# Kernel tuning notes

Measured on AMD Instinct MI355X. Metric: run time of the kernel, lower is better.

## Reference

```python
import jax, jax.numpy as jnp
import numpy as np
from jax import lax

H = 512
V = 32000
B = 64
S = 64
T = 32
TQ = 32
NUM_HOP = 3


def _p(key, shape, scale=0.05):
    return jax.random.normal(key, shape, dtype=jnp.float32) * scale


def setup_inputs() -> dict:
    key = jax.random.key(0)
    ks = jax.random.split(key, 20)
    inp = {}
    inp["contexts"] = jax.random.randint(ks[0], (B, S, T), 0, V)
    inp["questions"] = jax.random.randint(ks[1], (B, TQ), 0, V)
    inp["emb"] = _p(ks[2], (V, H), 1.0)
    # input module: bidirectional GRU (torch gate order r,z,n)
    inp["Wih_f"] = _p(ks[3], (3 * H, H)); inp["Whh_f"] = _p(ks[4], (3 * H, H))
    inp["bih_f"] = jnp.zeros((3 * H,), jnp.float32); inp["bhh_f"] = jnp.zeros((3 * H,), jnp.float32)
    inp["Wih_b"] = _p(ks[5], (3 * H, H)); inp["Whh_b"] = _p(ks[6], (3 * H, H))
    inp["bih_b"] = jnp.zeros((3 * H,), jnp.float32); inp["bhh_b"] = jnp.zeros((3 * H,), jnp.float32)
    # question module GRU
    inp["qWih"] = _p(ks[7], (3 * H, H)); inp["qWhh"] = _p(ks[8], (3 * H, H))
    inp["qbih"] = jnp.zeros((3 * H,), jnp.float32); inp["qbhh"] = jnp.zeros((3 * H,), jnp.float32)
    # attention GRU cell (note: source reuses br as both biases)
    inp["Wr"] = _p(ks[9], (H, H)); inp["Ur"] = _p(ks[10], (H, H)); inp["br"] = jnp.ones((H,), jnp.float32)
    inp["W"] = _p(ks[11], (H, H)); inp["U"] = _p(ks[12], (H, H))
    # episodic memory gate MLP + next-memory projection
    inp["z1_w"] = _p(ks[13], (H, 4 * H)); inp["z1_b"] = jnp.zeros((H,), jnp.float32)
    inp["z2_w"] = _p(ks[14], (1, H)); inp["z2_b"] = jnp.zeros((1,), jnp.float32)
    inp["nm_w"] = _p(ks[15], (H, 3 * H)); inp["nm_b"] = jnp.zeros((H,), jnp.float32)
    # answer module
    inp["ans_w"] = _p(ks[16], (V, 2 * H)); inp["ans_b"] = jnp.zeros((V,), jnp.float32)
    return inp


def _pos_enc(slen, elen):
    # l[s, e] = 1 - s/slen - (e/elen)*(1 - 2*s/slen); indexed by SENTENCE dim, as in source
    s = np.arange(slen, dtype=np.float64)[:, None]
    e = np.arange(elen, dtype=np.float64)[None, :]
    l = 1.0 - s / slen - (e / elen) * (1.0 - 2.0 * s / slen)
    return jnp.asarray(l, dtype=jnp.float32)  # (S, H)


def _gru(x, Wih, Whh, bih, bhh, reverse=False):
    # x: (B, T, H); torch nn.GRU math with gate order r, z, n
    Bn, Tn, Hn = x.shape
    h0 = jnp.zeros((Bn, Hn), x.dtype)

    def step(h, xt):
        gx = xt @ Wih.T + bih
        gh = h @ Whh.T + bhh
        xr, xz, xn = jnp.split(gx, 3, axis=-1)
        hr, hz, hn = jnp.split(gh, 3, axis=-1)
        r = jax.nn.sigmoid(xr + hr)
        z = jax.nn.sigmoid(xz + hz)
        n = jnp.tanh(xn + r * hn)
        h_new = (1.0 - z) * n + z * h
        return h_new, h_new

    h_last, hs = lax.scan(step, h0, jnp.swapaxes(x, 0, 1), reverse=reverse)
    return jnp.swapaxes(hs, 0, 1), h_last


def _dmn(emb, Wih_f, Whh_f, bih_f, bhh_f, Wih_b, Whh_b, bih_b, bhh_b,
         qWih, qWhh, qbih, qbhh, Wr, Ur, br, W, U,
         z1_w, z1_b, z2_w, z2_b, nm_w, nm_b, ans_w, ans_b,
         contexts, questions):
    emb0 = emb.at[0].set(0.0)  # padding_idx=0
    Bn, Sn, Tn = contexts.shape
    Hn = emb.shape[1]
    # ---- input module ----
    ce = emb0[contexts]                                   # (B,S,T,H)
    pe = _pos_enc(Sn, Hn)                                 # (S,H), broadcast over tokens (faithful)
    facts_in = jnp.sum(ce * pe[None, :, None, :], axis=2)  # (B,S,H)
    hf, _ = _gru(facts_in, Wih_f, Whh_f, bih_f, bhh_f, reverse=False)
    hb, _ = _gru(facts_in, Wih_b, Whh_b, bih_b, bhh_b, reverse=True)
    facts = hf + hb                                       # (B,S,H); dropout = identity (eval)
    # ---- question module ----
    _, q = _gru(emb0[questions], qWih, qWhh, qbih, qbhh)  # (B,H)
    # ---- episodic memory hops ----
    facts_t = jnp.swapaxes(facts, 0, 1)                   # (S,B,H)
    M = q
    for _ in range(NUM_HOP):
        qb = q[:, None, :]
        Mb = M[:, None, :]
        z = jnp.concatenate([facts * qb, facts * Mb,
                             jnp.abs(facts - qb), jnp.abs(facts - Mb)], axis=-1)  # (B,S,4H)
        g1 = jnp.tanh(z @ z1_w.T + z1_b)
        G = jax.nn.softmax((g1 @ z2_w.T + z2_b)[..., 0], axis=1)  # (B,S)

        def agru(c, sg):
            fact, g = sg
            r = jax.nn.sigmoid(fact @ Wr + c @ Ur + br)
            ht = jnp.tanh(fact @ W + r * (c @ U) + br)  # source reuses br as b
            return g[:, None] * ht + (1.0 - g[:, None]) * c, None

        C, _ = lax.scan(agru, jnp.zeros((Bn, Hn), facts.dtype), (facts_t, G.T))
        M = jax.nn.relu(jnp.concatenate([M, C, q], axis=-1) @ nm_w.T + nm_b)
    # ---- answer module (dropout = identity) ----
    preds = jnp.concatenate([M, q], axis=-1) @ ans_w.T + ans_b  # (B,V)
    return preds


def reference(contexts, questions, emb, Wih_f, Whh_f, bih_f, bhh_f,
              Wih_b, Whh_b, bih_b, bhh_b, qWih, qWhh, qbih, qbhh,
              Wr, Ur, br, W, U, z1_w, z1_b, z2_w, z2_b, nm_w, nm_b,
              ans_w, ans_b):
    return _dmn(emb, Wih_f, Whh_f, bih_f, bhh_f, Wih_b, Whh_b, bih_b, bhh_b,
                qWih, qWhh, qbih, qbhh, Wr, Ur, br, W, U,
                z1_w, z1_b, z2_w, z2_b, nm_w, nm_b, ans_w, ans_b,
                contexts, questions)
```

## Files before the change

kernel.cpp:

```cpp
#include <hip/hip_runtime.h>
#include <cstddef>
#include <cstdint>

namespace {

constexpr int H  = 512;
constexpr int V  = 32000;
constexpr int B  = 64;
constexpr int S  = 64;
constexpr int T  = 32;
constexpr int TQ = 32;

typedef unsigned short ushort_t;
typedef __attribute__((ext_vector_type(8))) short bf16x8;
typedef __attribute__((ext_vector_type(4))) short bf16x4;
typedef __attribute__((ext_vector_type(4))) float f32x4;

__device__ __forceinline__ ushort_t f2bf(float f) {
  union { float f; unsigned u; } v; v.f = f;
  return (ushort_t)((v.u + 0x7FFFu + ((v.u >> 16) & 1u)) >> 16);
}

__device__ __forceinline__ float sigm(float x) { return 1.f / (1.f + expf(-x)); }

__device__ __forceinline__ bf16x8 pack8(f32x4 a, f32x4 b) {
  bf16x8 r;
  r[0] = (short)f2bf(a.x); r[1] = (short)f2bf(a.y);
  r[2] = (short)f2bf(a.z); r[3] = (short)f2bf(a.w);
  r[4] = (short)f2bf(b.x); r[5] = (short)f2bf(b.y);
  r[6] = (short)f2bf(b.z); r[7] = (short)f2bf(b.w);
  return r;
}
__device__ __forceinline__ bf16x4 pack4(f32x4 a) {
  bf16x4 r;
  r[0] = (short)f2bf(a.x); r[1] = (short)f2bf(a.y);
  r[2] = (short)f2bf(a.z); r[3] = (short)f2bf(a.w);
  return r;
}

__device__ __forceinline__ f32x4 load4c(const float* p) {
  f32x4 v;
  asm volatile("global_load_dwordx4 %0, %1, off sc0 sc1" : "=v"(v) : "v"(p));
  return v;
}
__device__ __forceinline__ float load1c(const float* p) {
  float v;
  asm volatile("global_load_dword %0, %1, off sc0 sc1" : "=v"(v) : "v"(p));
  return v;
}
__device__ __forceinline__ void store1c(float* p, float v) {
  asm volatile("global_store_dword %0, %1, off sc0 sc1" :: "v"(p), "v"(v) : "memory");
}
__device__ __forceinline__ void waitvm0() {
  asm volatile("s_waitcnt vmcnt(0)" ::: "memory");
  __builtin_amdgcn_sched_barrier(0);
}

__device__ __forceinline__ void group_barrier_nc(unsigned* cell, unsigned target) {
  waitvm0();
  __syncthreads();
  if (threadIdx.x == 0) {
    __hip_atomic_fetch_add(cell, 1u, __ATOMIC_RELAXED, __HIP_MEMORY_SCOPE_AGENT);
    unsigned v;
    do {
      v = __hip_atomic_load(cell, __ATOMIC_RELAXED, __HIP_MEMORY_SCOPE_AGENT);
      if (v < target) __builtin_amdgcn_s_sleep(2);
    } while (v < target);
  }
  __syncthreads();
}

__global__ __launch_bounds__(256) void k_embed_facts(const int* __restrict__ ctx,
                                                     const float* __restrict__ emb,
                                                     float* __restrict__ facts_in) {
  const int bs = blockIdx.x;
  const int s  = bs & (S - 1);
  const int t  = threadIdx.x;
  __shared__ int sidx[T];
  if (t < T) sidx[t] = ctx[(size_t)bs * T + t];
  __syncthreads();
  float a0 = 0.f, a1 = 0.f;
  for (int tt = 0; tt < T; ++tt) {
    const int ix = sidx[tt];
    if (ix != 0) {
      const float* e = emb + ((size_t)ix << 9);
      a0 += e[t];
      a1 += e[t + 256];
    }
  }
  const float sf = (float)s * (1.f / 64.f);
  const float c1 = 1.f - sf;
  const float c2 = (1.f - 2.f * sf) * (1.f / 512.f);
  facts_in[((size_t)bs << 9) + t]       = a0 * (c1 - (float)t * c2);
  facts_in[((size_t)bs << 9) + t + 256] = a1 * (c1 - (float)(t + 256) * c2);
}

__global__ __launch_bounds__(256) void k_embed_q(const int* __restrict__ qidx,
                                                 const float* __restrict__ emb,
                                                 float* __restrict__ qe) {
  const int bt = blockIdx.x;
  const int t  = threadIdx.x;
  const int ix = qidx[bt];
  float v0 = 0.f, v1 = 0.f;
  if (ix != 0) {
    const float* e = emb + ((size_t)ix << 9);
    v0 = e[t];
    v1 = e[t + 256];
  }
  qe[((size_t)bt << 9) + t]       = v0;
  qe[((size_t)bt << 9) + t + 256] = v1;
}

__global__ __launch_bounds__(256) void k_transpose512(const float* __restrict__ src,
                                                      float* __restrict__ dst) {
  __shared__ float tile[32][33];
  const int x0 = blockIdx.x * 32, y0 = blockIdx.y * 32;
  for (int i = threadIdx.y; i < 32; i += 8)
    tile[i][threadIdx.x] = src[(size_t)(y0 + i) * H + x0 + threadIdx.x];
  __syncthreads();
  for (int i = threadIdx.y; i < 32; i += 8)
    dst[(size_t)(x0 + i) * H + y0 + threadIdx.x] = tile[threadIdx.x][i];
}

template <bool A_BF16, int ACT>
__global__ __launch_bounds__(256) void k_gemm_mfma(const void* __restrict__ Av,
                                                   const float* __restrict__ Bm,
                                                   const float* __restrict__ bias,
                                                   float* __restrict__ C,
                                                   int M, int N, int K) {
  __shared__ __align__(16) ushort_t As[64][72];
  __shared__ __align__(16) ushort_t Bs[64][72];
  const int t    = threadIdx.x;
  const int lane = t & 63;
  const int w    = t >> 6;
  const int wr   = w >> 1, wc = w & 1;
  const int m0 = blockIdx.y << 6, n0 = blockIdx.x << 6;
  const int row = t >> 2;
  const int ch  = t & 3;

  f32x4 acc[2][2] = {};

  for (int k0 = 0; k0 < K; k0 += 64) {
    if (A_BF16) {
      const ushort_t* A16 = (const ushort_t*)Av;
#pragma unroll
      for (int cc = 0; cc < 2; ++cc) {
        const int c8 = ch + cc * 4;
        const uint4 v = *(const uint4*)(A16 + (size_t)(m0 + row) * K + k0 + c8 * 8);
        *(uint4*)&As[row][c8 * 8] = v;
      }
    } else {
      const float* Af = (const float*)Av;
#pragma unroll
      for (int cc = 0; cc < 2; ++cc) {
        const int c8 = ch + cc * 4;
        const float* src = Af + (size_t)(m0 + row) * K + k0 + c8 * 8;
        const f32x4 f0 = *(const f32x4*)src;
        const f32x4 f1 = *(const f32x4*)(src + 4);
        *(bf16x8*)&As[row][c8 * 8] = pack8(f0, f1);
      }
    }
    {
#pragma unroll
      for (int cc = 0; cc < 2; ++cc) {
        const int c8 = ch + cc * 4;
        const float* src = Bm + (size_t)(n0 + row) * K + k0 + c8 * 8;
        const f32x4 f0 = *(const f32x4*)src;
        const f32x4 f1 = *(const f32x4*)(src + 4);
        *(bf16x8*)&Bs[row][c8 * 8] = pack8(f0, f1);
      }
    }
    __syncthreads();
#pragma unroll
    for (int ks = 0; ks < 2; ++ks) {
      bf16x8 a[2], b[2];
#pragma unroll
      for (int fr = 0; fr < 2; ++fr)
        a[fr] = *(const bf16x8*)&As[wr * 32 + fr * 16 + (lane & 15)][ks * 32 + (lane >> 4) * 8];
#pragma unroll
      for (int fc = 0; fc < 2; ++fc)
        b[fc] = *(const bf16x8*)&Bs[wc * 32 + fc * 16 + (lane & 15)][ks * 32 + (lane >> 4) * 8];
#pragma unroll
      for (int fr = 0; fr < 2; ++fr)
#pragma unroll
        for (int fc = 0; fc < 2; ++fc)
          acc[fr][fc] = __builtin_amdgcn_mfma_f32_16x16x32_bf16(a[fr], b[fc], acc[fr][fc], 0, 0, 0);
    }
    __syncthreads();
  }
#pragma unroll
  for (int fr = 0; fr < 2; ++fr) {
#pragma unroll
    for (int fc = 0; fc < 2; ++fc) {
      const int rbase = m0 + wr * 32 + fr * 16 + ((lane >> 4) << 2);
      const int col   = n0 + wc * 32 + fc * 16 + (lane & 15);
      const float bv  = bias ? bias[col] : 0.f;
#pragma unroll
      for (int j = 0; j < 4; ++j) {
        float v = acc[fr][fc][j] + bv;
        if (ACT == 1) v = tanhf(v);
        if (ACT == 2) v = fmaxf(v, 0.f);
        C[(size_t)(rbase + j) * N + col] = v;
      }
    }
  }
}

__global__ __launch_bounds__(256, 1) void k_gru_scan_mfma(
    const float* __restrict__ Whh_f, const float* __restrict__ bhh_f,
    const float* __restrict__ Whh_b, const float* __restrict__ bhh_b,
    const float* __restrict__ qWhh,  const float* __restrict__ qbhh,
    const float* __restrict__ gx_f, const float* __restrict__ gx_b,
    const float* __restrict__ gx_q,
    float* __restrict__ Hbuf, float* __restrict__ facts,
    float* __restrict__ hb_all, unsigned* __restrict__ bar) {
  const int bx   = blockIdx.x;
  const int grp  = bx >> 3;
  const int rank = bx & 7;
  const int gru  = grp >> 2;
  const int ib   = grp & 3;

  const float* Whh; const float* bhh; const float* gx;
  float* H0; float* H1; float* out_seq; int seqlen, rev;
  if (gru == 0)      { Whh = Whh_f; bhh = bhh_f; gx = gx_f; H0 = Hbuf;          H1 = Hbuf + 32768;  out_seq = facts;   seqlen = S;  rev = 0; }
  else if (gru == 1) { Whh = Whh_b; bhh = bhh_b; gx = gx_b; H0 = Hbuf + 65536;  H1 = Hbuf + 98304;  out_seq = hb_all;  seqlen = S;  rev = 1; }
  else               { Whh = qWhh;  bhh = qbhh;  gx = gx_q; H0 = Hbuf + 131072; H1 = Hbuf + 163840; out_seq = nullptr; seqlen = TQ; rev = 0; }

  __shared__ __align__(16) ushort_t hl[16 * 520];

  const int t    = threadIdx.x;
  const int lane = t & 63;
  const int wv   = t >> 6;
  const int nt   = (rank << 2) + wv;
  const int lm   = lane & 15;
  const int lk   = lane >> 4;
  const int col  = (nt << 4) + lm;

  bf16x8 wf[3][16];
#pragma unroll
  for (int g = 0; g < 3; ++g) {
    const float* wrow = Whh + ((size_t)(g * 512 + col) << 9) + (lk << 3);
#pragma unroll
    for (int ks = 0; ks < 16; ++ks) {
      const float* p = wrow + ks * 32;
      wf[g][ks] = pack8(*(const f32x4*)p, *(const f32x4*)(p + 4));
    }
  }
  const float bv0 = bhh[col], bv1 = bhh[512 + col], bv2 = bhh[1024 + col];
  unsigned* cell = bar + grp * 64;
  unsigned tgt = 0;

  for (int s = 0; s < seqlen; ++s) {
    const int xidx = rev ? (seqlen - 1 - s) : s;
    float xr[4], xz[4], xn[4];
#pragma unroll
    for (int j = 0; j < 4; ++j) {
      const int b = (ib << 4) + (lk << 2) + j;
      const size_t gxrow = ((size_t)b * seqlen + xidx) * 1536;
      xr[j] = gx[gxrow + col];
      xz[j] = gx[gxrow + 512 + col];
      xn[j] = gx[gxrow + 1024 + col];
    }

    float hp[4] = {0.f, 0.f, 0.f, 0.f};
    if (s == 0) {
      for (int i = t; i < 4160; i += 256) ((unsigned*)hl)[i] = 0u;
    } else {
      const float* Hp = (s & 1) ? H1 : H0;
      f32x4 v[8];
#pragma unroll
      for (int u = 0; u < 8; ++u) {
        const int i = (u << 8) + t;
        v[u] = load4c(Hp + ((size_t)((ib << 4) + (i >> 7)) << 9) + ((i & 127) << 2));
      }
#pragma unroll
      for (int j = 0; j < 4; ++j)
        hp[j] = load1c(Hp + ((size_t)((ib << 4) + (lk << 2) + j) << 9) + col);
      waitvm0();
#pragma unroll
      for (int u = 0; u < 8; ++u) {
        const int i = (u << 8) + t;
        *(bf16x4*)&hl[(i >> 7) * 520 + ((i & 127) << 2)] = pack4(v[u]);
      }
    }
    __syncthreads();

    f32x4 acc0 = {}, acc1 = {}, acc2 = {};
#pragma unroll
    for (int ks = 0; ks < 16; ++ks) {
      const bf16x8 a = *(const bf16x8*)&hl[lm * 520 + (ks << 5) + (lk << 3)];
      acc0 = __builtin_amdgcn_mfma_f32_16x16x32_bf16(a, wf[0][ks], acc0, 0, 0, 0);
      acc1 = __builtin_amdgcn_mfma_f32_16x16x32_bf16(a, wf[1][ks], acc1, 0, 0, 0);
      acc2 = __builtin_amdgcn_mfma_f32_16x16x32_bf16(a, wf[2][ks], acc2, 0, 0, 0);
    }

    float* Hn = (s & 1) ? H0 : H1;
#pragma unroll
    for (int j = 0; j < 4; ++j) {
      const int b = (ib << 4) + (lk << 2) + j;
      const float r = sigm(xr[j] + acc0[j] + bv0);
      const float z = sigm(xz[j] + acc1[j] + bv1);
      const float n = tanhf(xn[j] + r * (acc2[j] + bv2));
      const float hnew = (1.f - z) * n + z * hp[j];
      store1c(Hn + ((size_t)b << 9) + col, hnew);
      if (out_seq) out_seq[((size_t)(b * S + xidx) << 9) + col] = hnew;
    }
    if (s + 1 < seqlen) {
      tgt += 8;
      group_barrier_nc(cell, tgt);
    }
  }
}

__global__ __launch_bounds__(256, 1) void k_agru_scan_mfma(
    const float* __restrict__ UrT, const float* __restrict__ UT,
    const float* __restrict__ fRW, const float* __restrict__ fW,
    const float* __restrict__ br, const float* __restrict__ G,
    float* __restrict__ C0, float* __restrict__ C1,
    unsigned* __restrict__ bar) {
  const int bx   = blockIdx.x;
  const int grp  = bx >> 3;
  const int rank = bx & 7;

  __shared__ __align__(16) ushort_t cl[16 * 520];

  const int t    = threadIdx.x;
  const int lane = t & 63;
  const int wv   = t >> 6;
  const int nt   = (rank << 2) + wv;
  const int lm   = lane & 15;
  const int lk   = lane >> 4;
  const int col  = (nt << 4) + lm;

  bf16x8 wfr[16], wfu[16];
  {
    const float* r0 = UrT + ((size_t)col << 9) + (lk << 3);
    const float* r1 = UT  + ((size_t)col << 9) + (lk << 3);
#pragma unroll
    for (int ks = 0; ks < 16; ++ks) {
      wfr[ks] = pack8(*(const f32x4*)(r0 + ks * 32), *(const f32x4*)(r0 + ks * 32 + 4));
      wfu[ks] = pack8(*(const f32x4*)(r1 + ks * 32), *(const f32x4*)(r1 + ks * 32 + 4));
    }
  }
  const float brv = br[col];
  unsigned* cell = bar + grp * 64;
  unsigned tgt = 0;

  for (int s = 0; s < S; ++s) {
    float fr[4], fw[4], gg[4];
#pragma unroll
    for (int j = 0; j < 4; ++j) {
      const int b = (grp << 4) + (lk << 2) + j;
      const size_t fi = ((size_t)(b * S + s) << 9) + col;
      fr[j] = fRW[fi];
      fw[j] = fW[fi];
      gg[j] = G[(b << 6) + s];
    }

    float cp[4] = {0.f, 0.f, 0.f, 0.f};
    if (s == 0) {
      for (int i = t; i < 4160; i += 256) ((unsigned*)cl)[i] = 0u;
    } else {
      const float* Cp = (s & 1) ? C1 : C0;
      f32x4 v[8];
#pragma unroll
      for (int u = 0; u < 8; ++u) {
        const int i = (u << 8) + t;
        v[u] = load4c(Cp + ((size_t)((grp << 4) + (i >> 7)) << 9) + ((i & 127) << 2));
      }
#pragma unroll
      for (int j = 0; j < 4; ++j)
        cp[j] = load1c(Cp + ((size_t)((grp << 4) + (lk << 2) + j) << 9) + col);
      waitvm0();
#pragma unroll
      for (int u = 0; u < 8; ++u) {
        const int i = (u << 8) + t;
        *(bf16x4*)&cl[(i >> 7) * 520 + ((i & 127) << 2)] = pack4(v[u]);
      }
    }
    __syncthreads();

    f32x4 accr = {}, accu = {};
#pragma unroll
    for (int ks = 0; ks < 16; ++ks) {
      const bf16x8 a = *(const bf16x8*)&cl[lm * 520 + (ks << 5) + (lk << 3)];
      accr = __builtin_amdgcn_mfma_f32_16x16x32_bf16(a, wfr[ks], accr, 0, 0, 0);
      accu = __builtin_amdgcn_mfma_f32_16x16x32_bf16(a, wfu[ks], accu, 0, 0, 0);
    }

    float* Cn = (s & 1) ? C0 : C1;
#pragma unroll
    for (int j = 0; j < 4; ++j) {
      const int b = (grp << 4) + (lk << 2) + j;
      const float r  = sigm(fr[j] + accr[j] + brv);
      const float ht = tanhf(fw[j] + r * accu[j] + brv);
      store1c(Cn + ((size_t)b << 9) + col, gg[j] * ht + (1.f - gg[j]) * cp[j]);
    }
    if (s + 1 < S) {
      tgt += 8;
      group_barrier_nc(cell, tgt);
    }
  }
}

__global__ __launch_bounds__(256) void k_add(float* __restrict__ a, const float* __restrict__ b) {
  const size_t i = (((size_t)blockIdx.x << 8) + threadIdx.x) << 2;
  float4 x = *(float4*)(a + i);
  const float4 y = *(const float4*)(b + i);
  x.x += y.x; x.y += y.y; x.z += y.z; x.w += y.w;
  *(float4*)(a + i) = x;
}

__global__ __launch_bounds__(256) void k_build_z16(const float* __restrict__ facts,
                                                   const float* __restrict__ q,
                                                   const float* __restrict__ M,
                                                   ushort_t* __restrict__ z) {
  const int bs = blockIdx.x;
  const int b  = bs >> 6;
  const int t  = threadIdx.x;
  const size_t zb = (size_t)bs << 11;
  for (int c = t; c < 512; c += 256) {
    const float f  = facts[((size_t)bs << 9) + c];
    const float qv = q[(b << 9) + c];
    const float mv = M[(b << 9) + c];
    z[zb + c]        = f2bf(f * qv);
    z[zb + 512 + c]  = f2bf(f * mv);
    z[zb + 1024 + c] = f2bf(fabsf(f - qv));
    z[zb + 1536 + c] = f2bf(fabsf(f - mv));
  }
}

__global__ __launch_bounds__(256) void k_score_softmax(const float* __restrict__ g1,
                                                       const float* __restrict__ z2w,
                                                       const float* __restrict__ z2b,
                                                       float* __restrict__ G) {
  const int b = blockIdx.x, t = threadIdx.x;
  const int wave = t >> 6, lane = t & 63;
  __shared__ float sc[64];
  for (int si = 0; si < 16; ++si) {
    const int s = wave * 16 + si;
    const float* row = g1 + ((size_t)(b * S + s) << 9) + lane * 8;
    const float* w   = z2w + lane * 8;
    float p = 0.f;
#pragma unroll
    for (int k = 0; k < 8; ++k) p += row[k] * w[k];
#pragma unroll
    for (int off = 32; off; off >>= 1) p += __shfl_xor(p, off);
    if (lane == 0) sc[s] = p + z2b[0];
  }
  __syncthreads();
  if (wave == 0) {
    const float v = sc[lane];
    float m = v;
#pragma unroll
    for (int off = 32; off; off >>= 1) m = fmaxf(m, __shfl_xor(m, off));
    const float e = expf(v - m);
    float su = e;
#pragma unroll
    for (int off = 32; off; off >>= 1) su += __shfl_xor(su, off);
    G[(b << 6) + lane] = e / su;
  }
}

__global__ __launch_bounds__(256) void k_concat3(const float* __restrict__ M,
                                                 const float* __restrict__ C,
                                                 const float* __restrict__ q,
                                                 float* __restrict__ out) {
  const int b = blockIdx.x, t = threadIdx.x;
  for (int c = t; c < 512; c += 256) {
    out[(size_t)b * 1536 + c]        = M[(b << 9) + c];
    out[(size_t)b * 1536 + 512 + c]  = C[(b << 9) + c];
    out[(size_t)b * 1536 + 1024 + c] = q[(b << 9) + c];
  }
}

__global__ __launch_bounds__(256) void k_concat2(const float* __restrict__ M,
                                                 const float* __restrict__ q,
                                                 float* __restrict__ out) {
  const int b = blockIdx.x, t = threadIdx.x;
  for (int c = t; c < 512; c += 256) {
    out[(size_t)b * 1024 + c]       = M[(b << 9) + c];
    out[(size_t)b * 1024 + 512 + c] = q[(b << 9) + c];
  }
}

}

extern "C" void kernel_launch(void* const* d_in, const int* in_sizes, int n_in,
                              void* d_out, int out_size, void* d_ws, size_t ws_size,
                              hipStream_t stream) {
  const int*   contexts  = (const int*)d_in[0];
  const int*   questions = (const int*)d_in[1];
  const float* emb   = (const float*)d_in[2];
  const float* Wih_f = (const float*)d_in[3];
  const float* Whh_f = (const float*)d_in[4];
  const float* bih_f = (const float*)d_in[5];
  const float* bhh_f = (const float*)d_in[6];
  const float* Wih_b = (const float*)d_in[7];
  const float* Whh_b = (const float*)d_in[8];
  const float* bih_b = (const float*)d_in[9];
  const float* bhh_b = (const float*)d_in[10];
  const float* qWih  = (const float*)d_in[11];
  const float* qWhh  = (const float*)d_in[12];
  const float* qbih  = (const float*)d_in[13];
  const float* qbhh  = (const float*)d_in[14];
  const float* Wr    = (const float*)d_in[15];
  const float* Ur    = (const float*)d_in[16];
  const float* br    = (const float*)d_in[17];
  const float* Wm    = (const float*)d_in[18];
  const float* Um    = (const float*)d_in[19];
  const float* z1_w  = (const float*)d_in[20];
  const float* z1_b  = (const float*)d_in[21];
  const float* z2_w  = (const float*)d_in[22];
  const float* z2_b  = (const float*)d_in[23];
  const float* nm_w  = (const float*)d_in[24];
  const float* nm_b  = (const float*)d_in[25];
  const float* ans_w = (const float*)d_in[26];
  const float* ans_b = (const float*)d_in[27];
  (void)in_sizes; (void)n_in; (void)out_size; (void)ws_size;

  float* ws = (float*)d_ws;
  float* WrT      = ws + 0;
  float* UrT      = ws + 262144;
  float* WT       = ws + 524288;
  float* UT       = ws + 786432;
  float* facts_in = ws + 1048576;
  float* qe       = ws + 3145728;
  float* gx_f     = ws + 4194304;
  float* gx_b     = ws + 10485760;
  float* gx_q     = ws + 16777216;
  float* facts    = ws + 19922944;
  float* hb       = ws + 22020096;
  float* Hbuf     = ws + 24117248;
  float* C0       = ws + 24313856;
  float* C1       = ws + 24346624;
  float* M0       = ws + 24379392;
  float* M1       = ws + 24412160;
  float* MCq      = ws + 24444928;
  float* Mq       = ws + 24543232;
  float* Gm       = ws + 24608768;
  ushort_t* zb16 = (ushort_t*)gx_f;
  float* g1  = gx_q;
  float* fRW = facts_in;
  float* fW  = hb;
  float* preds = (float*)d_out;
  unsigned* bar = (unsigned*)Mq;

  float* Hq0 = Hbuf + 131072;
  float* q = Hq0;

  hipMemsetAsync(bar, 0, 48 * 64 * sizeof(unsigned), stream);

  k_embed_facts<<<B * S, 256, 0, stream>>>(contexts, emb, facts_in);
  k_embed_q<<<B * TQ, 256, 0, stream>>>(questions, emb, qe);
  dim3 tb(32, 8);
  k_transpose512<<<dim3(16, 16), tb, 0, stream>>>(Wr, WrT);
  k_transpose512<<<dim3(16, 16), tb, 0, stream>>>(Ur, UrT);
  k_transpose512<<<dim3(16, 16), tb, 0, stream>>>(Wm, WT);
  k_transpose512<<<dim3(16, 16), tb, 0, stream>>>(Um, UT);

  k_gemm_mfma<false, 0><<<dim3(24, 64), 256, 0, stream>>>(facts_in, Wih_f, bih_f, gx_f, 4096, 1536, 512);
  k_gemm_mfma<false, 0><<<dim3(24, 64), 256, 0, stream>>>(facts_in, Wih_b, bih_b, gx_b, 4096, 1536, 512);
  k_gemm_mfma<false, 0><<<dim3(24, 32), 256, 0, stream>>>(qe, qWih, qbih, gx_q, 2048, 1536, 512);

  k_gru_scan_mfma<<<96, 256, 0, stream>>>(Whh_f, bhh_f, Whh_b, bhh_b, qWhh, qbhh,
                                          gx_f, gx_b, gx_q, Hbuf, facts, hb, bar);
  k_add<<<2048, 256, 0, stream>>>(facts, hb);

  k_gemm_mfma<false, 0><<<dim3(8, 64), 256, 0, stream>>>(facts, WrT, nullptr, fRW, 4096, 512, 512);
  k_gemm_mfma<false, 0><<<dim3(8, 64), 256, 0, stream>>>(facts, WT,  nullptr, fW,  4096, 512, 512);

  const float* Mcur = q;
  for (int h = 0; h < 3; ++h) {
    k_build_z16<<<B * S, 256, 0, stream>>>(facts, q, Mcur, zb16);
    k_gemm_mfma<true, 1><<<dim3(8, 64), 256, 0, stream>>>(zb16, z1_w, z1_b, g1, 4096, 512, 2048);
    k_score_softmax<<<B, 256, 0, stream>>>(g1, z2_w, z2_b, Gm);
    {
      unsigned* ba = bar + (24 + h * 8) * 64;
      k_agru_scan_mfma<<<32, 256, 0, stream>>>(UrT, UT, fRW, fW, br, Gm, C0, C1, ba);
    }
    k_concat3<<<B, 256, 0, stream>>>(Mcur, C0, q, MCq);
    float* Mnext = (h & 1) ? M1 : M0;
    k_gemm_mfma<false, 2><<<dim3(8, 1), 256, 0, stream>>>(MCq, nm_w, nm_b, Mnext, 64, 512, 1536);
    Mcur = Mnext;
  }

  k_concat2<<<B, 256, 0, stream>>>(Mcur, q, Mq);
  k_gemm_mfma<false, 0><<<dim3(500, 1), 256, 0, stream>>>(Mq, ans_w, ans_b, preds, 64, 32000, 1024);
}
```

Measured before the change: 1.462 ms.

## Use per-rank flag barriers, prefetch next-step inputs, fuse concat/z-build into GEMMs

Replaces the atomic-counter group barrier in both GRU scans with per-rank flag stores polled by one wavefront, which removes contended atomics on the serial critical path. Next-step gate inputs are loaded before the barrier so their latency overlaps the wait. The z-feature build, concat3 and concat2 kernels are folded into specialized GEMM loaders, cutting launches and intermediate buffers. The trade-off is that z1 now recomputes the elementwise features per N-tile.

```diff
diff --git a/kernel.cpp b/kernel.cpp
--- a/kernel.cpp
+++ b/kernel.cpp
@@ -25,16 +25,16 @@
 
 __device__ __forceinline__ bf16x8 pack8(f32x4 a, f32x4 b) {
   bf16x8 r;
-  r[0] = (short)f2bf(a.x); r[1] = (short)f2bf(a.y);
-  r[2] = (short)f2bf(a.z); r[3] = (short)f2bf(a.w);
-  r[4] = (short)f2bf(b.x); r[5] = (short)f2bf(b.y);
-  r[6] = (short)f2bf(b.z); r[7] = (short)f2bf(b.w);
+  r[0] = (short)f2bf(a[0]); r[1] = (short)f2bf(a[1]);
+  r[2] = (short)f2bf(a[2]); r[3] = (short)f2bf(a[3]);
+  r[4] = (short)f2bf(b[0]); r[5] = (short)f2bf(b[1]);
+  r[6] = (short)f2bf(b[2]); r[7] = (short)f2bf(b[3]);
   return r;
 }
 __device__ __forceinline__ bf16x4 pack4(f32x4 a) {
   bf16x4 r;
-  r[0] = (short)f2bf(a.x); r[1] = (short)f2bf(a.y);
-  r[2] = (short)f2bf(a.z); r[3] = (short)f2bf(a.w);
+  r[0] = (short)f2bf(a[0]); r[1] = (short)f2bf(a[1]);
+  r[2] = (short)f2bf(a[2]); r[3] = (short)f2bf(a[3]);
   return r;
 }
 
@@ -51,21 +51,29 @@
 __device__ __forceinline__ void store1c(float* p, float v) {
   asm volatile("global_store_dword %0, %1, off sc0 sc1" :: "v"(p), "v"(v) : "memory");
 }
+__device__ __forceinline__ void store1cu(unsigned* p, unsigned v) {
+  asm volatile("global_store_dword %0, %1, off sc0 sc1" :: "v"(p), "v"(v) : "memory");
+}
 __device__ __forceinline__ void waitvm0() {
   asm volatile("s_waitcnt vmcnt(0)" ::: "memory");
   __builtin_amdgcn_sched_barrier(0);
 }
 
-__device__ __forceinline__ void group_barrier_nc(unsigned* cell, unsigned target) {
+__device__ __forceinline__ void flag_barrier(unsigned* flags, int rank,
+                                             unsigned step1, int t, int lane, int wv) {
   waitvm0();
   __syncthreads();
-  if (threadIdx.x == 0) {
-    __hip_atomic_fetch_add(cell, 1u, __ATOMIC_RELAXED, __HIP_MEMORY_SCOPE_AGENT);
-    unsigned v;
-    do {
-      v = __hip_atomic_load(cell, __ATOMIC_RELAXED, __HIP_MEMORY_SCOPE_AGENT);
-      if (v < target) __builtin_amdgcn_s_sleep(2);
-    } while (v < target);
+  if (t == 0) store1cu(flags + rank * 32, step1);
+  if (wv == 0) {
+    const unsigned* fp = flags + (lane & 7) * 32;
+    for (;;) {
+      unsigned v;
+      asm volatile("global_load_dword %0, %1, off sc0 sc1" : "=v"(v) : "v"(fp));
+      asm volatile("s_waitcnt vmcnt(0)" ::: "memory");
+      const int ok = (lane >= 8) || (v >= step1);
+      if (__all(ok)) break;
+      __builtin_amdgcn_s_sleep(1);
+    }
   }
   __syncthreads();
 }
@@ -122,8 +130,8 @@
     dst[(size_t)(x0 + i) * H + y0 + threadIdx.x] = tile[threadIdx.x][i];
 }
 
-template <bool A_BF16, int ACT>
-__global__ __launch_bounds__(256) void k_gemm_mfma(const void* __restrict__ Av,
+template <int ACT>
+__global__ __launch_bounds__(256) void k_gemm_mfma(const float* __restrict__ Af,
                                                    const float* __restrict__ Bm,
                                                    const float* __restrict__ bias,
                                                    float* __restrict__ C,
@@ -141,34 +149,13 @@
   f32x4 acc[2][2] = {};
 
   for (int k0 = 0; k0 < K; k0 += 64) {
-    if (A_BF16) {
-      const ushort_t* A16 = (const ushort_t*)Av;
-#pragma unroll
-      for (int cc = 0; cc < 2; ++cc) {
-        const int c8 = ch + cc * 4;
-        const uint4 v = *(const uint4*)(A16 + (size_t)(m0 + row) * K + k0 + c8 * 8);
-        *(uint4*)&As[row][c8 * 8] = v;
-      }
-    } else {
-      const float* Af = (const float*)Av;
-#pragma unroll
-      for (int cc = 0; cc < 2; ++cc) {
-        const int c8 = ch + cc * 4;
-        const float* src = Af + (size_t)(m0 + row) * K + k0 + c8 * 8;
-        const f32x4 f0 = *(const f32x4*)src;
-        const f32x4 f1 = *(const f32x4*)(src + 4);
-        *(bf16x8*)&As[row][c8 * 8] = pack8(f0, f1);
-      }
-    }
-    {
-#pragma unroll
-      for (int cc = 0; cc < 2; ++cc) {
-        const int c8 = ch + cc * 4;
-        const float* src = Bm + (size_t)(n0 + row) * K + k0 + c8 * 8;
-        const f32x4 f0 = *(const f32x4*)src;
-        const f32x4 f1 = *(const f32x4*)(src + 4);
-        *(bf16x8*)&Bs[row][c8 * 8] = pack8(f0, f1);
-      }
+#pragma unroll
+    for (int cc = 0; cc < 2; ++cc) {
+      const int c8 = ch + cc * 4;
+      const float* src = Af + (size_t)(m0 + row) * K + k0 + c8 * 8;
+      *(bf16x8*)&As[row][c8 * 8] = pack8(*(const f32x4*)src, *(const f32x4*)(src + 4));
+      const float* srb = Bm + (size_t)(n0 + row) * K + k0 + c8 * 8;
+      *(bf16x8*)&Bs[row][c8 * 8] = pack8(*(const f32x4*)srb, *(const f32x4*)(srb + 4));
     }
     __syncthreads();
 #pragma unroll
@@ -202,6 +189,207 @@
         if (ACT == 2) v = fmaxf(v, 0.f);
         C[(size_t)(rbase + j) * N + col] = v;
       }
+    }
+  }
+}
+
+__global__ __launch_bounds__(256) void k_gemm_z1(const float* __restrict__ facts,
+                                                 const float* __restrict__ qv,
+                                                 const float* __restrict__ Mv,
+                                                 const float* __restrict__ Bm,
+                                                 const float* __restrict__ bias,
+                                                 float* __restrict__ C) {
+  constexpr int N = 512, K = 2048;
+  __shared__ __align__(16) ushort_t As[64][72];
+  __shared__ __align__(16) ushort_t Bs[64][72];
+  const int t    = threadIdx.x;
+  const int lane = t & 63;
+  const int w    = t >> 6;
+  const int wr   = w >> 1, wc = w & 1;
+  const int m0 = blockIdx.y << 6, n0 = blockIdx.x << 6;
+  const int row = t >> 2;
+  const int ch  = t & 3;
+  const int b   = blockIdx.y;
+
+  f32x4 acc[2][2] = {};
+
+  for (int k0 = 0; k0 < K; k0 += 64) {
+    const int seg = k0 >> 9;
+    const int kb  = k0 & 511;
+    const float* other = ((seg & 1) ? Mv : qv) + ((size_t)b << 9);
+#pragma unroll
+    for (int cc = 0; cc < 2; ++cc) {
+      const int c8 = ch + cc * 4;
+      const int kk = kb + c8 * 8;
+      const float* fp = facts + ((size_t)(m0 + row) << 9) + kk;
+      const f32x4 f0 = *(const f32x4*)fp;
+      const f32x4 f1 = *(const f32x4*)(fp + 4);
+      const f32x4 o0 = *(const f32x4*)(other + kk);
+      const f32x4 o1 = *(const f32x4*)(other + kk + 4);
+      f32x4 z0, z1;
+      if (seg < 2) {
+        z0 = f0 * o0; z1 = f1 * o1;
+      } else {
+        z0 = f0 - o0; z1 = f1 - o1;
+#pragma unroll
+        for (int e = 0; e < 4; ++e) { z0[e] = fabsf(z0[e]); z1[e] = fabsf(z1[e]); }
+      }
+      *(bf16x8*)&As[row][c8 * 8] = pack8(z0, z1);
+      const float* srb = Bm + (size_t)(n0 + row) * K + k0 + c8 * 8;
+      *(bf16x8*)&Bs[row][c8 * 8] = pack8(*(const f32x4*)srb, *(const f32x4*)(srb + 4));
+    }
+    __syncthreads();
+#pragma unroll
+    for (int ks = 0; ks < 2; ++ks) {
+      bf16x8 a[2], bb[2];
+#pragma unroll
+      for (int fr = 0; fr < 2; ++fr)
+        a[fr] = *(const bf16x8*)&As[wr * 32 + fr * 16 + (lane & 15)][ks * 32 + (lane >> 4) * 8];
+#pragma unroll
+      for (int fc = 0; fc < 2; ++fc)
+        bb[fc] = *(const bf16x8*)&Bs[wc * 32 + fc * 16 + (lane & 15)][ks * 32 + (lane >> 4) * 8];
+#pragma unroll
+      for (int fr = 0; fr < 2; ++fr)
+#pragma unroll
+        for (int fc = 0; fc < 2; ++fc)
+          acc[fr][fc] = __builtin_amdgcn_mfma_f32_16x16x32_bf16(a[fr], bb[fc], acc[fr][fc], 0, 0, 0);
+    }
+    __syncthreads();
+  }
+#pragma unroll
+  for (int fr = 0; fr < 2; ++fr) {
+#pragma unroll
+    for (int fc = 0; fc < 2; ++fc) {
+      const int rbase = m0 + wr * 32 + fr * 16 + ((lane >> 4) << 2);
+      const int col   = n0 + wc * 32 + fc * 16 + (lane & 15);
+      const float bv  = bias[col];
+#pragma unroll
+      for (int j = 0; j < 4; ++j)
+        C[(size_t)(rbase + j) * N + col] = tanhf(acc[fr][fc][j] + bv);
+    }
+  }
+}
+
+__global__ __launch_bounds__(256) void k_gemm_cat3(const float* __restrict__ Mv,
+                                                   const float* __restrict__ Cv,
+                                                   const float* __restrict__ qv,
+                                                   const float* __restrict__ Bm,
+                                                   const float* __restrict__ bias,
+                                                   float* __restrict__ C) {
+  constexpr int N = 512, K = 1536;
+  __shared__ __align__(16) ushort_t As[64][72];
+  __shared__ __align__(16) ushort_t Bs[64][72];
+  const int t    = threadIdx.x;
+  const int lane = t & 63;
+  const int w    = t >> 6;
+  const int wr   = w >> 1, wc = w & 1;
+  const int n0 = blockIdx.x << 6;
+  const int row = t >> 2;
+  const int ch  = t & 3;
+
+  f32x4 acc[2][2] = {};
+
+  for (int k0 = 0; k0 < K; k0 += 64) {
+    const int seg = k0 >> 9;
+    const float* src = (seg == 0) ? Mv : (seg == 1) ? Cv : qv;
+    const int kb = k0 & 511;
+#pragma unroll
+    for (int cc = 0; cc < 2; ++cc) {
+      const int c8 = ch + cc * 4;
+      const float* fp = src + ((size_t)row << 9) + kb + c8 * 8;
+      *(bf16x8*)&As[row][c8 * 8] = pack8(*(const f32x4*)fp, *(const f32x4*)(fp + 4));
+      const float* srb = Bm + (size_t)(n0 + row) * K + k0 + c8 * 8;
+      *(bf16x8*)&Bs[row][c8 * 8] = pack8(*(const f32x4*)srb, *(const f32x4*)(srb + 4));
+    }
+    __syncthreads();
+#pragma unroll
+    for (int ks = 0; ks < 2; ++ks) {
+      bf16x8 a[2], bb[2];
+#pragma unroll
+      for (int fr = 0; fr < 2; ++fr)
+        a[fr] = *(const bf16x8*)&As[wr * 32 + fr * 16 + (lane & 15)][ks * 32 + (lane >> 4) * 8];
+#pragma unroll
+      for (int fc = 0; fc < 2; ++fc)
+        bb[fc] = *(const bf16x8*)&Bs[wc * 32 + fc * 16 + (lane & 15)][ks * 32 + (lane >> 4) * 8];
+#pragma unroll
+      for (int fr = 0; fr < 2; ++fr)
+#pragma unroll
+        for (int fc = 0; fc < 2; ++fc)
+          acc[fr][fc] = __builtin_amdgcn_mfma_f32_16x16x32_bf16(a[fr], bb[fc], acc[fr][fc], 0, 0, 0);
+    }
+    __syncthreads();
+  }
+#pragma unroll
+  for (int fr = 0; fr < 2; ++fr) {
+#pragma unroll
+    for (int fc = 0; fc < 2; ++fc) {
+      const int rbase = wr * 32 + fr * 16 + ((lane >> 4) << 2);
+      const int col   = n0 + wc * 32 + fc * 16 + (lane & 15);
+      const float bv  = bias[col];
+#pragma unroll
+      for (int j = 0; j < 4; ++j)
+        C[(size_t)(rbase + j) * N + col] = fmaxf(acc[fr][fc][j] + bv, 0.f);
+    }
+  }
+}
+
+__global__ __launch_bounds__(256) void k_gemm_cat2(const float* __restrict__ Mv,
+                                                   const float* __restrict__ qv,
+                                                   const float* __restrict__ Bm,
+                                                   const float* __restrict__ bias,
+                                                   float* __restrict__ C) {
+  constexpr int N = 32000, K = 1024;
+  __shared__ __align__(16) ushort_t As[64][72];
+  __shared__ __align__(16) ushort_t Bs[64][72];
+  const int t    = threadIdx.x;
+  const int lane = t & 63;
+  const int w    = t >> 6;
+  const int wr   = w >> 1, wc = w & 1;
+  const int n0 = blockIdx.x << 6;
+  const int row = t >> 2;
+  const int ch  = t & 3;
+
+  f32x4 acc[2][2] = {};
+
+  for (int k0 = 0; k0 < K; k0 += 64) {
+    const float* src = (k0 < 512) ? Mv : qv;
+    const int kb = k0 & 511;
+#pragma unroll
+    for (int cc = 0; cc < 2; ++cc) {
+      const int c8 = ch + cc * 4;
+      const float* fp = src + ((size_t)row << 9) + kb + c8 * 8;
+      *(bf16x8*)&As[row][c8 * 8] = pack8(*(const f32x4*)fp, *(const f32x4*)(fp + 4));
+      const float* srb = Bm + (size_t)(n0 + row) * K + k0 + c8 * 8;
+      *(bf16x8*)&Bs[row][c8 * 8] = pack8(*(const f32x4*)srb, *(const f32x4*)(srb + 4));
+    }
+    __syncthreads();
+#pragma unroll
+    for (int ks = 0; ks < 2; ++ks) {
+      bf16x8 a[2], bb[2];
+#pragma unroll
+      for (int fr = 0; fr < 2; ++fr)
+        a[fr] = *(const bf16x8*)&As[wr * 32 + fr * 16 + (lane & 15)][ks * 32 + (lane >> 4) * 8];
+#pragma unroll
+      for (int fc = 0; fc < 2; ++fc)
+        bb[fc] = *(const bf16x8*)&Bs[wc * 32 + fc * 16 + (lane & 15)][ks * 32 + (lane >> 4) * 8];
+#pragma unroll
+      for (int fr = 0; fr < 2; ++fr)
+#pragma unroll
+        for (int fc = 0; fc < 2; ++fc)
+          acc[fr][fc] = __builtin_amdgcn_mfma_f32_16x16x32_bf16(a[fr], bb[fc], acc[fr][fc], 0, 0, 0);
+    }
+    __syncthreads();
+  }
+#pragma unroll
+  for (int fr = 0; fr < 2; ++fr) {
+#pragma unroll
+    for (int fc = 0; fc < 2; ++fc) {
+      const int rbase = wr * 32 + fr * 16 + ((lane >> 4) << 2);
+      const int col   = n0 + wc * 32 + fc * 16 + (lane & 15);
+      const float bv  = bias[col];
+#pragma unroll
+      for (int j = 0; j < 4; ++j)
+        C[(size_t)(rbase + j) * N + col] = acc[fr][fc][j] + bv;
     }
   }
 }
@@ -213,7 +401,7 @@
     const float* __restrict__ gx_f, const float* __restrict__ gx_b,
     const float* __restrict__ gx_q,
     float* __restrict__ Hbuf, float* __restrict__ facts,
-    float* __restrict__ hb_all, unsigned* __restrict__ bar) {
+    float* __restrict__ hb_all, unsigned* __restrict__ flags_base) {
   const int bx   = blockIdx.x;
   const int grp  = bx >> 3;
   const int rank = bx & 7;
@@ -247,12 +435,11 @@
     }
   }
   const float bv0 = bhh[col], bv1 = bhh[512 + col], bv2 = bhh[1024 + col];
-  unsigned* cell = bar + grp * 64;
-  unsigned tgt = 0;
-
-  for (int s = 0; s < seqlen; ++s) {
-    const int xidx = rev ? (seqlen - 1 - s) : s;
-    float xr[4], xz[4], xn[4];
+  unsigned* flags = flags_base + grp * 8 * 32;
+
+  float xr[4], xz[4], xn[4];
+  {
+    const int xidx = rev ? (seqlen - 1) : 0;
 #pragma unroll
     for (int j = 0; j < 4; ++j) {
       const int b = (ib << 4) + (lk << 2) + j;
@@ -261,7 +448,9 @@
       xz[j] = gx[gxrow + 512 + col];
       xn[j] = gx[gxrow + 1024 + col];
     }
-
+  }
+
+  for (int s = 0; s < seqlen; ++s) {
     float hp[4] = {0.f, 0.f, 0.f, 0.f};
     if (s == 0) {
       for (int i = t; i < 4160; i += 256) ((unsigned*)hl)[i] = 0u;
@@ -294,6 +483,7 @@
       acc2 = __builtin_amdgcn_mfma_f32_16x16x32_bf16(a, wf[2][ks], acc2, 0, 0, 0);
     }
 
+    const int xidx = rev ? (seqlen - 1 - s) : s;
     float* Hn = (s & 1) ? H0 : H1;
 #pragma unroll
     for (int j = 0; j < 4; ++j) {
@@ -305,9 +495,21 @@
       store1c(Hn + ((size_t)b << 9) + col, hnew);
       if (out_seq) out_seq[((size_t)(b * S + xidx) << 9) + col] = hnew;
     }
+
     if (s + 1 < seqlen) {
-      tgt += 8;
-      group_barrier_nc(cell, tgt);
+      const int xidx2 = rev ? (seqlen - 2 - s) : (s + 1);
+      float nxr[4], nxz[4], nxn[4];
+#pragma unroll
+      for (int j = 0; j < 4; ++j) {
+        const int b = (ib << 4) + (lk << 2) + j;
+        const size_t gxrow = ((size_t)b * seqlen + xidx2) * 1536;
+        nxr[j] = gx[gxrow + col];
+        nxz[j] = gx[gxrow + 512 + col];
+        nxn[j] = gx[gxrow + 1024 + col];
+      }
+      flag_barrier(flags, rank, (unsigned)(s + 1), t, lane, wv);
+#pragma unroll
+      for (int j = 0; j < 4; ++j) { xr[j] = nxr[j]; xz[j] = nxz[j]; xn[j] = nxn[j]; }
     }
   }
 }
@@ -317,7 +519,7 @@
     const float* __restrict__ fRW, const float* __restrict__ fW,
     const float* __restrict__ br, const float* __restrict__ G,
     float* __restrict__ C0, float* __restrict__ C1,
-    unsigned* __restrict__ bar) {
+    unsigned* __restrict__ flags_base) {
   const int bx   = blockIdx.x;
   const int grp  = bx >> 3;
   const int rank = bx & 7;
@@ -343,20 +545,19 @@
     }
   }
   const float brv = br[col];
-  unsigned* cell = bar + grp * 64;
-  unsigned tgt = 0;
+  unsigned* flags = flags_base + grp * 8 * 32;
+
+  float fr[4], fw[4], gg[4];
+#pragma unroll
+  for (int j = 0; j < 4; ++j) {
+    const int b = (grp << 4) + (lk << 2) + j;
+    const size_t fi = ((size_t)(b * S) << 9) + col;
+    fr[j] = fRW[fi];
+    fw[j] = fW[fi];
+    gg[j] = G[b << 6];
+  }
 
   for (int s = 0; s < S; ++s) {
-    float fr[4], fw[4], gg[4];
-#pragma unroll
-    for (int j = 0; j < 4; ++j) {
-      const int b = (grp << 4) + (lk << 2) + j;
-      const size_t fi = ((size_t)(b * S + s) << 9) + col;
-      fr[j] = fRW[fi];
-      fw[j] = fW[fi];
-      gg[j] = G[(b << 6) + s];
-    }
-
     float cp[4] = {0.f, 0.f, 0.f, 0.f};
     if (s == 0) {
       for (int i = t; i < 4160; i += 256) ((unsigned*)cl)[i] = 0u;
@@ -396,9 +597,20 @@
       const float ht = tanhf(fw[j] + r * accu[j] + brv);
       store1c(Cn + ((size_t)b << 9) + col, gg[j] * ht + (1.f - gg[j]) * cp[j]);
     }
+
     if (s + 1 < S) {
-      tgt += 8;
-      group_barrier_nc(cell, tgt);
+      float nfr[4], nfw[4], ngg[4];
+#pragma unroll
+      for (int j = 0; j < 4; ++j) {
+        const int b = (grp << 4) + (lk << 2) + j;
+        const size_t fi = ((size_t)(b * S + s + 1) << 9) + col;
+        nfr[j] = fRW[fi];
+        nfw[j] = fW[fi];
+        ngg[j] = G[(b << 6) + s + 1];
+      }
+      flag_barrier(flags, rank, (unsigned)(s + 1), t, lane, wv);
+#pragma unroll
+      for (int j = 0; j < 4; ++j) { fr[j] = nfr[j]; fw[j] = nfw[j]; gg[j] = ngg[j]; }
     }
   }
 }
@@ -409,25 +621,6 @@
   const float4 y = *(const float4*)(b + i);
   x.x += y.x; x.y += y.y; x.z += y.z; x.w += y.w;
   *(float4*)(a + i) = x;
-}
-
-__global__ __launch_bounds__(256) void k_build_z16(const float* __restrict__ facts,
-                                                   const float* __restrict__ q,
-                                                   const float* __restrict__ M,
-                                                   ushort_t* __restrict__ z) {
-  const int bs = blockIdx.x;
-  const int b  = bs >> 6;
-  const int t  = threadIdx.x;
-  const size_t zb = (size_t)bs << 11;
-  for (int c = t; c < 512; c += 256) {
-    const float f  = facts[((size_t)bs << 9) + c];
-    const float qv = q[(b << 9) + c];
-    const float mv = M[(b << 9) + c];
-    z[zb + c]        = f2bf(f * qv);
-    z[zb + 512 + c]  = f2bf(f * mv);
-    z[zb + 1024 + c] = f2bf(fabsf(f - qv));
-    z[zb + 1536 + c] = f2bf(fabsf(f - mv));
-  }
 }
 
 __global__ __launch_bounds__(256) void k_score_softmax(const float* __restrict__ g1,
@@ -459,28 +652,6 @@
 #pragma unroll
     for (int off = 32; off; off >>= 1) su += __shfl_xor(su, off);
     G[(b << 6) + lane] = e / su;
-  }
-}
-
-__global__ __launch_bounds__(256) void k_concat3(const float* __restrict__ M,
-                                                 const float* __restrict__ C,
-                                                 const float* __restrict__ q,
-                                                 float* __restrict__ out) {
-  const int b = blockIdx.x, t = threadIdx.x;
-  for (int c = t; c < 512; c += 256) {
-    out[(size_t)b * 1536 + c]        = M[(b << 9) + c];
-    out[(size_t)b * 1536 + 512 + c]  = C[(b << 9) + c];
-    out[(size_t)b * 1536 + 1024 + c] = q[(b << 9) + c];
-  }
-}
-
-__global__ __launch_bounds__(256) void k_concat2(const float* __restrict__ M,
-                                                 const float* __restrict__ q,
-                                                 float* __restrict__ out) {
-  const int b = blockIdx.x, t = threadIdx.x;
-  for (int c = t; c < 512; c += 256) {
-    out[(size_t)b * 1024 + c]       = M[(b << 9) + c];
-    out[(size_t)b * 1024 + 512 + c] = q[(b << 9) + c];
   }
 }
 
@@ -536,20 +707,17 @@
   float* C1       = ws + 24346624;
   float* M0       = ws + 24379392;
   float* M1       = ws + 24412160;
-  float* MCq      = ws + 24444928;
   float* Mq       = ws + 24543232;
   float* Gm       = ws + 24608768;
-  ushort_t* zb16 = (ushort_t*)gx_f;
   float* g1  = gx_q;
   float* fRW = facts_in;
   float* fW  = hb;
   float* preds = (float*)d_out;
   unsigned* bar = (unsigned*)Mq;
 
-  float* Hq0 = Hbuf + 131072;
-  float* q = Hq0;
-
-  hipMemsetAsync(bar, 0, 48 * 64 * sizeof(unsigned), stream);
+  float* q = Hbuf + 131072;
+
+  hipMemsetAsync(bar, 0, 6144 * sizeof(unsigned), stream);
 
   k_embed_facts<<<B * S, 256, 0, stream>>>(contexts, emb, facts_in);
   k_embed_q<<<B * TQ, 256, 0, stream>>>(questions, emb, qe);
@@ -559,32 +727,27 @@
   k_transpose512<<<dim3(16, 16), tb, 0, stream>>>(Wm, WT);
   k_transpose512<<<dim3(16, 16), tb, 0, stream>>>(Um, UT);
 
-  k_gemm_mfma<false, 0><<<dim3(24, 64), 256, 0, stream>>>(facts_in, Wih_f, bih_f, gx_f, 4096, 1536, 512);
-  k_gemm_mfma<false, 0><<<dim3(24, 64), 256, 0, stream>>>(facts_in, Wih_b, bih_b, gx_b, 4096, 1536, 512);
-  k_gemm_mfma<false, 0><<<dim3(24, 32), 256, 0, stream>>>(qe, qWih, qbih, gx_q, 2048, 1536, 512);
+  k_gemm_mfma<0><<<dim3(24, 64), 256, 0, stream>>>(facts_in, Wih_f, bih_f, gx_f, 4096, 1536, 512);
+  k_gemm_mfma<0><<<dim3(24, 64), 256, 0, stream>>>(facts_in, Wih_b, bih_b, gx_b, 4096, 1536, 512);
+  k_gemm_mfma<0><<<dim3(24, 32), 256, 0, stream>>>(qe, qWih, qbih, gx_q, 2048, 1536, 512);
 
   k_gru_scan_mfma<<<96, 256, 0, stream>>>(Whh_f, bhh_f, Whh_b, bhh_b, qWhh, qbhh,
                                           gx_f, gx_b, gx_q, Hbuf, facts, hb, bar);
   k_add<<<2048, 256, 0, stream>>>(facts, hb);
 
-  k_gemm_mfma<false, 0><<<dim3(8, 64), 256, 0, stream>>>(facts, WrT, nullptr, fRW, 4096, 512, 512);
-  k_gemm_mfma<false, 0><<<dim3(8, 64), 256, 0, stream>>>(facts, WT,  nullptr, fW,  4096, 512, 512);
+  k_gemm_mfma<0><<<dim3(8, 64), 256, 0, stream>>>(facts, WrT, nullptr, fRW, 4096, 512, 512);
+  k_gemm_mfma<0><<<dim3(8, 64), 256, 0, stream>>>(facts, WT,  nullptr, fW,  4096, 512, 512);
 
   const float* Mcur = q;
   for (int h = 0; h < 3; ++h) {
-    k_build_z16<<<B * S, 256, 0, stream>>>(facts, q, Mcur, zb16);
-    k_gemm_mfma<true, 1><<<dim3(8, 64), 256, 0, stream>>>(zb16, z1_w, z1_b, g1, 4096, 512, 2048);
+    k_gemm_z1<<<dim3(8, 64), 256, 0, stream>>>(facts, q, Mcur, z1_w, z1_b, g1);
     k_score_softmax<<<B, 256, 0, stream>>>(g1, z2_w, z2_b, Gm);
-    {
-      unsigned* ba = bar + (24 + h * 8) * 64;
-      k_agru_scan_mfma<<<32, 256, 0, stream>>>(UrT, UT, fRW, fW, br, Gm, C0, C1, ba);
-    }
-    k_concat3<<<B, 256, 0, stream>>>(Mcur, C0, q, MCq);
+    unsigned* fl = bar + 3072 + h * 1024;
+    k_agru_scan_mfma<<<32, 256, 0, stream>>>(UrT, UT, fRW, fW, br, Gm, C0, C1, fl);
     float* Mnext = (h & 1) ? M1 : M0;
-    k_gemm_mfma<false, 2><<<dim3(8, 1), 256, 0, stream>>>(MCq, nm_w, nm_b, Mnext, 64, 512, 1536);
+    k_gemm_cat3<<<dim3(8, 1), 256, 0, stream>>>(Mcur, C0, q, nm_w, nm_b, Mnext);
     Mcur = Mnext;
   }
 
-  k_concat2<<<B, 256, 0, stream>>>(Mcur, q, Mq);
-  k_gemm_mfma<false, 0><<<dim3(500, 1), 256, 0, stream>>>(Mq, ans_w, ans_b, preds, 64, 32000, 1024);
-}
+  k_gemm_cat2<<<dim3(500, 1), 256, 0, stream>>>(Mcur, q, ans_w, ans_b, preds);
+}
```

Result: slower. 1.585 ms (+8.4%).
